# Kernel tuning notes

Measured on AMD Instinct MI355X. Metric: run time of the kernel, lower is better.

The kernel has to match this reference:

```python
import jax, jax.numpy as jnp
import numpy as np

TEMPERATURE = 0.07
N_CLASSES = 100


def setup_inputs() -> dict:
    key = jax.random.key(0)
    k1, k2 = jax.random.split(key)
    N, D = 8192, 128
    emb = jax.random.normal(k1, (N, D), dtype=jnp.float32)
    # unit-normalize so exp(sim / temperature) stays finite in fp32
    emb = emb / jnp.linalg.norm(emb, axis=1, keepdims=True)
    labels = jax.random.randint(k2, (N,), 0, N_CLASSES, dtype=jnp.int64)
    return {"embeddings": emb, "labels": labels}


def reference(embeddings, labels):
    N = embeddings.shape[0]
    dt = embeddings.dtype
    # [N, N] similarity
    sim = jnp.matmul(embeddings, embeddings.T) / TEMPERATURE
    off_diag = 1.0 - jnp.eye(N, dtype=dt)
    pos_mask = (labels[:, None] == labels[None, :]).astype(dt) * off_diag
    exp_sim = jnp.exp(sim) * off_diag  # diagonal zeroed
    positive_sum = jnp.sum(exp_sim * pos_mask, axis=1)
    total_sum = jnp.sum(exp_sim, axis=1)
    loss = -jnp.log(positive_sum / (total_sum + 1e-8) + 1e-8)
    valid = pos_mask.sum(axis=1) > 0
    cnt = jnp.sum(valid.astype(dt))
    mean_loss = jnp.where(
        cnt > 0,
        jnp.sum(jnp.where(valid, loss, jnp.zeros_like(loss))) / jnp.maximum(cnt, 1.0),
        jnp.asarray(0.0, dtype=dt),
    )
    return mean_loss
```

## Files before the change

### kernel.cpp

```cpp
#include <hip/hip_runtime.h>

#define N 8192
#define D 128
#define SCALE_A 20.6098592f
#define NBX 64
#define NBY 8
#define NBLK (NBX * NBY)

using short8  = __attribute__((ext_vector_type(8))) short;
using float4v = __attribute__((ext_vector_type(4))) float;

#if __has_builtin(__builtin_amdgcn_exp2f)
#define EXP2(x) __builtin_amdgcn_exp2f(x)
#else
#define EXP2(x) __expf((x) * 0.69314718f)
#endif

static __device__ inline unsigned int f2bf(float f) {
    union { float f; unsigned int u; } x;
    x.f = f;
    unsigned int u = x.u;
    return (u + 0x7FFFu + ((u >> 16) & 1u)) >> 16;
}

__global__ __launch_bounds__(256) void cl_prep(
    const float* __restrict__ emb, unsigned short* __restrict__ bfB,
    unsigned short* __restrict__ bfA, float* __restrict__ tot,
    int* __restrict__ ticket)
{
    const int t = blockIdx.x * 256 + threadIdx.x;
    const float* p = emb + (size_t)t * 16;
    uint4 ob[2], oa[2];
    #pragma unroll
    for (int h = 0; h < 2; ++h) {
        float4v f0 = *(const float4v*)(p + h * 8);
        float4v f1 = *(const float4v*)(p + h * 8 + 4);
        ob[h].x = f2bf(f0[0]) | (f2bf(f0[1]) << 16);
        ob[h].y = f2bf(f0[2]) | (f2bf(f0[3]) << 16);
        ob[h].z = f2bf(f1[0]) | (f2bf(f1[1]) << 16);
        ob[h].w = f2bf(f1[2]) | (f2bf(f1[3]) << 16);
        oa[h].x = f2bf(f0[0] * SCALE_A) | (f2bf(f0[1] * SCALE_A) << 16);
        oa[h].y = f2bf(f0[2] * SCALE_A) | (f2bf(f0[3] * SCALE_A) << 16);
        oa[h].z = f2bf(f1[0] * SCALE_A) | (f2bf(f1[1] * SCALE_A) << 16);
        oa[h].w = f2bf(f1[2] * SCALE_A) | (f2bf(f1[3] * SCALE_A) << 16);
    }
    ((uint4*)bfB)[t * 2]     = ob[0];
    ((uint4*)bfB)[t * 2 + 1] = ob[1];
    ((uint4*)bfA)[t * 2]     = oa[0];
    ((uint4*)bfA)[t * 2 + 1] = oa[1];
    if (t < 2 * N) tot[t] = 0.f;
    if (t == 0) *ticket = 0;
}

__global__ __launch_bounds__(256, 2) void cl_main(
    const unsigned short* __restrict__ bfA, const unsigned short* __restrict__ bfB,
    const int* __restrict__ labels,
    float* __restrict__ tot, float* __restrict__ pos,
    int* __restrict__ ticket, float* __restrict__ out)
{
    __shared__ uint4 ldsB[128 * 16];
    __shared__ float sred[2][4];
    __shared__ int s_ticket;

    const int tid  = threadIdx.x;
    const int lane = tid & 63;
    const int wave = tid >> 6;
    const int q    = lane >> 4;
    const int c    = lane & 15;
    const int rw   = blockIdx.x * 128 + wave * 32;

    short8 afrag[2][4];
    int rowlab[2][4];
    #pragma unroll
    for (int tr = 0; tr < 2; ++tr) {
        const int arow = rw + tr * 16 + c;
        #pragma unroll
        for (int ks = 0; ks < 4; ++ks)
            afrag[tr][ks] = *(const short8*)(bfA + (size_t)arow * D + ks * 32 + q * 8);
        #pragma unroll
        for (int reg = 0; reg < 4; ++reg)
            rowlab[tr][reg] = labels[rw + tr * 16 + q * 4 + reg];
    }

    float tot_a[2][4] = {{0.f,0.f,0.f,0.f},{0.f,0.f,0.f,0.f}};
    float pos_a[2][4] = {{0.f,0.f,0.f,0.f},{0.f,0.f,0.f,0.f}};

    for (int it = 0; it < 8; ++it) {
        const int cbase = blockIdx.y * 1024 + it * 128;

        const uint4* bfB4 = (const uint4*)bfB;
        #pragma unroll
        for (int i = 0; i < 8; ++i) {
            const int g     = tid + i * 256;
            const int brow  = g >> 4;
            const int chunk = g & 15;
            uint4 u = bfB4[(size_t)(cbase + brow) * 16 + chunk];
            ldsB[brow * 16 + (chunk ^ (brow & 15))] = u;
        }
        int collab[8];
        #pragma unroll
        for (int tc = 0; tc < 8; ++tc) collab[tc] = labels[cbase + tc * 16 + c];
        __syncthreads();

        float4v acc[2][8];
        #pragma unroll
        for (int tr = 0; tr < 2; ++tr)
            #pragma unroll
            for (int tc = 0; tc < 8; ++tc) {
                float4v z = {0.f, 0.f, 0.f, 0.f};
                acc[tr][tc] = z;
            }

        const short8* ldsS = (const short8*)ldsB;
        #pragma unroll
        for (int ks = 0; ks < 4; ++ks) {
            const short8* pk = ldsS + c * 16 + ((ks * 4 + q) ^ c);
            #pragma unroll
            for (int tc = 0; tc < 8; ++tc) {
                short8 b = pk[tc * 256];
                #pragma unroll
                for (int tr = 0; tr < 2; ++tr)
                    acc[tr][tc] = __builtin_amdgcn_mfma_f32_16x16x32_bf16(
                        afrag[tr][ks], b, acc[tr][tc], 0, 0, 0);
            }
        }

        #pragma unroll
        for (int tr = 0; tr < 2; ++tr) {
            const int rtile = rw + tr * 16;
            #pragma unroll
            for (int tc = 0; tc < 8; ++tc) {
                const bool diag_tile = (rtile == cbase + tc * 16);
                const int lc = collab[tc];
                #pragma unroll
                for (int reg = 0; reg < 4; ++reg) {
                    float v = EXP2(acc[tr][tc][reg]);
                    if (diag_tile && (q * 4 + reg) == c) v = 0.f;
                    tot_a[tr][reg] += v;
                    if (rowlab[tr][reg] == lc) pos_a[tr][reg] += v;
                }
            }
        }
        __syncthreads();
    }

    #pragma unroll
    for (int tr = 0; tr < 2; ++tr)
        #pragma unroll
        for (int reg = 0; reg < 4; ++reg) {
            float t = tot_a[tr][reg];
            float p = pos_a[tr][reg];
            #pragma unroll
            for (int m = 1; m < 16; m <<= 1) {
                t += __shfl_xor(t, m, 64);
                p += __shfl_xor(p, m, 64);
            }
            if (c == 0) {
                const int r = rw + tr * 16 + q * 4 + reg;
                atomicAdd(&tot[r], t);
                atomicAdd(&pos[r], p);
            }
        }

    asm volatile("s_waitcnt vmcnt(0)" ::: "memory");
    __syncthreads();
    if (tid == 0)
        s_ticket = __hip_atomic_fetch_add(ticket, 1, __ATOMIC_RELAXED,
                                          __HIP_MEMORY_SCOPE_AGENT);
    __syncthreads();
    if (s_ticket != NBLK - 1) return;

    float lsum = 0.f, lcnt = 0.f;
    #pragma unroll 4
    for (int i = tid; i < N; i += 256) {
        const float t = __hip_atomic_load(&tot[i], __ATOMIC_RELAXED,
                                          __HIP_MEMORY_SCOPE_AGENT);
        const float p = __hip_atomic_load(&pos[i], __ATOMIC_RELAXED,
                                          __HIP_MEMORY_SCOPE_AGENT);
        const float loss = -__logf(p / (t + 1e-8f) + 1e-8f);
        if (p > 0.f) { lsum += loss; lcnt += 1.f; }
    }
    #pragma unroll
    for (int m = 1; m < 64; m <<= 1) {
        lsum += __shfl_xor(lsum, m, 64);
        lcnt += __shfl_xor(lcnt, m, 64);
    }
    if (lane == 0) { sred[0][wave] = lsum; sred[1][wave] = lcnt; }
    __syncthreads();
    if (tid == 0) {
        const float s = sred[0][0] + sred[0][1] + sred[0][2] + sred[0][3];
        const float n = sred[1][0] + sred[1][1] + sred[1][2] + sred[1][3];
        out[0] = (n > 0.f) ? s / fmaxf(n, 1.f) : 0.f;
    }
}

extern "C" void kernel_launch(void* const* d_in, const int* in_sizes, int n_in,
                              void* d_out, int out_size, void* d_ws, size_t ws_size,
                              hipStream_t stream) {
    const float* emb  = (const float*)d_in[0];
    const int* labels = (const int*)d_in[1];
    unsigned short* bfB = (unsigned short*)d_ws;
    unsigned short* bfA = bfB + (size_t)N * D;
    float* tot    = (float*)(bfA + (size_t)N * D);
    float* pos    = tot + N;
    int*   ticket = (int*)(pos + N);

    cl_prep<<<256, 256, 0, stream>>>(emb, bfB, bfA, tot, ticket);
    cl_main<<<dim3(NBX, NBY), 256, 0, stream>>>(bfA, bfB, labels, tot, pos,
                                                ticket, (float*)d_out);
}
```

Baseline: 93.08 us.

## Double-buffer B tiles via direct global-to-LDS loads and stage column labels in LDS

Replaces the register round-trip B-tile staging with global_load_lds async copies into a double-buffered LDS tile, prefetching the next tile while the current one is multiplied and exponentiated. Column labels for the block's whole 1024-column span are loaded once into shared memory instead of being fetched from global every iteration. The change relies on manual vmcnt waits and raw s_barrier calls, which adds correctness risk around LDS visibility, and the extra LDS use may lower occupancy.

```diff
diff --git a/kernel.cpp b/kernel.cpp
--- a/kernel.cpp
+++ b/kernel.cpp
@@ -52,22 +52,43 @@
     if (t == 0) *ticket = 0;
 }
 
+static __device__ __forceinline__ void stage_tile(
+    const uint4* __restrict__ bfB4, int cbase, uint4* lds_dst, int tid)
+{
+    const uint4* src = bfB4 + (size_t)cbase * 16;
+    #pragma unroll
+    for (int i = 0; i < 8; ++i) {
+        const int g     = tid + i * 256;
+        const int row   = g >> 4;
+        const int chunk = g & 15;
+        __builtin_amdgcn_global_load_lds(
+            (const __attribute__((address_space(1))) void*)(src + row * 16 + (chunk ^ (row & 15))),
+            (__attribute__((address_space(3))) void*)(lds_dst + g),
+            16, 0, 0);
+    }
+}
+
 __global__ __launch_bounds__(256, 2) void cl_main(
     const unsigned short* __restrict__ bfA, const unsigned short* __restrict__ bfB,
     const int* __restrict__ labels,
     float* __restrict__ tot, float* __restrict__ pos,
     int* __restrict__ ticket, float* __restrict__ out)
 {
-    __shared__ uint4 ldsB[128 * 16];
+    __shared__ uint4 ldsB[2][128 * 16];
+    __shared__ int   s_collab[1024];
     __shared__ float sred[2][4];
-    __shared__ int s_ticket;
+    __shared__ int   s_ticket;
 
     const int tid  = threadIdx.x;
     const int lane = tid & 63;
     const int wave = tid >> 6;
     const int q    = lane >> 4;
     const int c    = lane & 15;
-    const int rw   = blockIdx.x * 128 + wave * 32;
+    const int rw     = blockIdx.x * 128 + wave * 32;
+    const int cbase0 = blockIdx.y * 1024;
+    const uint4* bfB4 = (const uint4*)bfB;
+
+    stage_tile(bfB4, cbase0, &ldsB[0][0], tid);
 
     short8 afrag[2][4];
     int rowlab[2][4];
@@ -82,25 +103,31 @@
             rowlab[tr][reg] = labels[rw + tr * 16 + q * 4 + reg];
     }
 
+    {
+        int4 lv = *(const int4*)(labels + cbase0 + tid * 4);
+        *(int4*)(&s_collab[tid * 4]) = lv;
+    }
+    asm volatile("s_waitcnt lgkmcnt(0)" ::: "memory");
+    __builtin_amdgcn_s_barrier();
+
     float tot_a[2][4] = {{0.f,0.f,0.f,0.f},{0.f,0.f,0.f,0.f}};
     float pos_a[2][4] = {{0.f,0.f,0.f,0.f},{0.f,0.f,0.f,0.f}};
 
+    int cur = 0;
+    #pragma unroll 1
     for (int it = 0; it < 8; ++it) {
-        const int cbase = blockIdx.y * 1024 + it * 128;
-
-        const uint4* bfB4 = (const uint4*)bfB;
-        #pragma unroll
-        for (int i = 0; i < 8; ++i) {
-            const int g     = tid + i * 256;
-            const int brow  = g >> 4;
-            const int chunk = g & 15;
-            uint4 u = bfB4[(size_t)(cbase + brow) * 16 + chunk];
-            ldsB[brow * 16 + (chunk ^ (brow & 15))] = u;
-        }
+        if (it < 7) {
+            stage_tile(bfB4, cbase0 + (it + 1) * 128, &ldsB[cur ^ 1][0], tid);
+            asm volatile("s_waitcnt vmcnt(8)" ::: "memory");
+        } else {
+            asm volatile("s_waitcnt vmcnt(0)" ::: "memory");
+        }
+        __builtin_amdgcn_s_barrier();
+        __builtin_amdgcn_sched_barrier(0);
+
         int collab[8];
         #pragma unroll
-        for (int tc = 0; tc < 8; ++tc) collab[tc] = labels[cbase + tc * 16 + c];
-        __syncthreads();
+        for (int tc = 0; tc < 8; ++tc) collab[tc] = s_collab[it * 128 + tc * 16 + c];
 
         float4v acc[2][8];
         #pragma unroll
@@ -111,7 +138,7 @@
                 acc[tr][tc] = z;
             }
 
-        const short8* ldsS = (const short8*)ldsB;
+        const short8* ldsS = (const short8*)&ldsB[cur][0];
         #pragma unroll
         for (int ks = 0; ks < 4; ++ks) {
             const short8* pk = ldsS + c * 16 + ((ks * 4 + q) ^ c);
@@ -125,6 +152,7 @@
             }
         }
 
+        const int cbase = cbase0 + it * 128;
         #pragma unroll
         for (int tr = 0; tr < 2; ++tr) {
             const int rtile = rw + tr * 16;
@@ -141,7 +169,10 @@
                 }
             }
         }
-        __syncthreads();
+
+        __builtin_amdgcn_sched_barrier(0);
+        __builtin_amdgcn_s_barrier();
+        cur ^= 1;
     }
 
     #pragma unroll
```

Result: no change. 93.37 us (+0.3%).

## Pre-swizzle bf16 operands into MFMA fragment layout and drop LDS staging

Applied to the files above, without the earlier changes.

The prep kernel now writes the bf16 A and B matrices in the exact per-lane MFMA fragment order, so the main kernel can load B fragments straight from global/L2 with coalesced short8 loads. The LDS tile, its swizzle and both barriers per iteration go away. The grid becomes 1024 one-dimensional blocks with 4 blocks per CU, each sweeping 32 column tiles of 16. The diagonal check moves to per-tile branches. Reuse of B drops from the whole block to a single wave, which raises L2 traffic, and the smaller accumulator set lowers per-wave ILP.

```diff
diff --git a/kernel.cpp b/kernel.cpp
--- a/kernel.cpp
+++ b/kernel.cpp
@@ -3,9 +3,8 @@
 #define N 8192
 #define D 128
 #define SCALE_A 20.6098592f
-#define NBX 64
-#define NBY 8
-#define NBLK (NBX * NBY)
+#define NBLK 1024
+#define NBLK_PREP 256
 
 using short8  = __attribute__((ext_vector_type(8))) short;
 using float4v = __attribute__((ext_vector_type(4))) float;
@@ -24,124 +23,144 @@
 }
 
 __global__ __launch_bounds__(256) void cl_prep(
-    const float* __restrict__ emb, unsigned short* __restrict__ bfB,
-    unsigned short* __restrict__ bfA, float* __restrict__ tot,
+    const float* __restrict__ emb, unsigned short* __restrict__ bfA,
+    unsigned short* __restrict__ bfB, float* __restrict__ tot,
     int* __restrict__ ticket)
 {
-    const int t = blockIdx.x * 256 + threadIdx.x;
-    const float* p = emb + (size_t)t * 16;
-    uint4 ob[2], oa[2];
-    #pragma unroll
-    for (int h = 0; h < 2; ++h) {
-        float4v f0 = *(const float4v*)(p + h * 8);
-        float4v f1 = *(const float4v*)(p + h * 8 + 4);
-        ob[h].x = f2bf(f0[0]) | (f2bf(f0[1]) << 16);
-        ob[h].y = f2bf(f0[2]) | (f2bf(f0[3]) << 16);
-        ob[h].z = f2bf(f1[0]) | (f2bf(f1[1]) << 16);
-        ob[h].w = f2bf(f1[2]) | (f2bf(f1[3]) << 16);
-        oa[h].x = f2bf(f0[0] * SCALE_A) | (f2bf(f0[1] * SCALE_A) << 16);
-        oa[h].y = f2bf(f0[2] * SCALE_A) | (f2bf(f0[3] * SCALE_A) << 16);
-        oa[h].z = f2bf(f1[0] * SCALE_A) | (f2bf(f1[1] * SCALE_A) << 16);
-        oa[h].w = f2bf(f1[2] * SCALE_A) | (f2bf(f1[3] * SCALE_A) << 16);
-    }
-    ((uint4*)bfB)[t * 2]     = ob[0];
-    ((uint4*)bfB)[t * 2 + 1] = ob[1];
-    ((uint4*)bfA)[t * 2]     = oa[0];
-    ((uint4*)bfA)[t * 2 + 1] = oa[1];
+    const int t  = blockIdx.x * 256 + threadIdx.x;
+    const int r  = t >> 3;
+    const int s  = t & 7;
+    const int ks = s >> 1;
+    const int h  = s & 1;
+    const int rt = r >> 4;
+    const int c  = r & 15;
+    const int base = (rt * 4 + ks) * 64 + h * 32 + c;
+
+    const float* p = emb + (size_t)r * D + s * 16;
+    float4v f0 = *(const float4v*)(p);
+    float4v f1 = *(const float4v*)(p + 4);
+    float4v f2 = *(const float4v*)(p + 8);
+    float4v f3 = *(const float4v*)(p + 12);
+
+    uint4 b0, b1, a0, a1;
+    b0.x = f2bf(f0[0]) | (f2bf(f0[1]) << 16);
+    b0.y = f2bf(f0[2]) | (f2bf(f0[3]) << 16);
+    b0.z = f2bf(f1[0]) | (f2bf(f1[1]) << 16);
+    b0.w = f2bf(f1[2]) | (f2bf(f1[3]) << 16);
+    b1.x = f2bf(f2[0]) | (f2bf(f2[1]) << 16);
+    b1.y = f2bf(f2[2]) | (f2bf(f2[3]) << 16);
+    b1.z = f2bf(f3[0]) | (f2bf(f3[1]) << 16);
+    b1.w = f2bf(f3[2]) | (f2bf(f3[3]) << 16);
+    a0.x = f2bf(f0[0] * SCALE_A) | (f2bf(f0[1] * SCALE_A) << 16);
+    a0.y = f2bf(f0[2] * SCALE_A) | (f2bf(f0[3] * SCALE_A) << 16);
+    a0.z = f2bf(f1[0] * SCALE_A) | (f2bf(f1[1] * SCALE_A) << 16);
+    a0.w = f2bf(f1[2] * SCALE_A) | (f2bf(f1[3] * SCALE_A) << 16);
+    a1.x = f2bf(f2[0] * SCALE_A) | (f2bf(f2[1] * SCALE_A) << 16);
+    a1.y = f2bf(f2[2] * SCALE_A) | (f2bf(f2[3] * SCALE_A) << 16);
+    a1.z = f2bf(f3[0] * SCALE_A) | (f2bf(f3[1] * SCALE_A) << 16);
+    a1.w = f2bf(f3[2] * SCALE_A) | (f2bf(f3[3] * SCALE_A) << 16);
+
+    ((uint4*)bfA)[base]      = a0;
+    ((uint4*)bfA)[base + 16] = a1;
+    ((uint4*)bfB)[base]      = b0;
+    ((uint4*)bfB)[base + 16] = b1;
+
     if (t < 2 * N) tot[t] = 0.f;
     if (t == 0) *ticket = 0;
 }
 
-__global__ __launch_bounds__(256, 2) void cl_main(
+__global__ __launch_bounds__(256, 4) void cl_main(
     const unsigned short* __restrict__ bfA, const unsigned short* __restrict__ bfB,
     const int* __restrict__ labels,
     float* __restrict__ tot, float* __restrict__ pos,
     int* __restrict__ ticket, float* __restrict__ out)
 {
-    __shared__ uint4 ldsB[128 * 16];
     __shared__ float sred[2][4];
-    __shared__ int s_ticket;
+    __shared__ int   s_ticket;
 
     const int tid  = threadIdx.x;
     const int lane = tid & 63;
     const int wave = tid >> 6;
     const int q    = lane >> 4;
     const int c    = lane & 15;
-    const int rw   = blockIdx.x * 128 + wave * 32;
+
+    const int rb = blockIdx.x & 63;
+    const int cs = blockIdx.x >> 6;
+    const int w0  = rb * 128 + wave * 32;
+    const int rt0 = w0 >> 4;
+    const int ct0 = cs * 32;
+
+    const short8* A8 = (const short8*)bfA;
+    const short8* B8 = (const short8*)bfB;
 
     short8 afrag[2][4];
     int rowlab[2][4];
     #pragma unroll
     for (int tr = 0; tr < 2; ++tr) {
-        const int arow = rw + tr * 16 + c;
         #pragma unroll
         for (int ks = 0; ks < 4; ++ks)
-            afrag[tr][ks] = *(const short8*)(bfA + (size_t)arow * D + ks * 32 + q * 8);
+            afrag[tr][ks] = A8[((rt0 + tr) * 4 + ks) * 64 + lane];
         #pragma unroll
         for (int reg = 0; reg < 4; ++reg)
-            rowlab[tr][reg] = labels[rw + tr * 16 + q * 4 + reg];
+            rowlab[tr][reg] = labels[w0 + tr * 16 + q * 4 + reg];
     }
 
     float tot_a[2][4] = {{0.f,0.f,0.f,0.f},{0.f,0.f,0.f,0.f}};
     float pos_a[2][4] = {{0.f,0.f,0.f,0.f},{0.f,0.f,0.f,0.f}};
 
-    for (int it = 0; it < 8; ++it) {
-        const int cbase = blockIdx.y * 1024 + it * 128;
-
-        const uint4* bfB4 = (const uint4*)bfB;
-        #pragma unroll
-        for (int i = 0; i < 8; ++i) {
-            const int g     = tid + i * 256;
-            const int brow  = g >> 4;
-            const int chunk = g & 15;
-            uint4 u = bfB4[(size_t)(cbase + brow) * 16 + chunk];
-            ldsB[brow * 16 + (chunk ^ (brow & 15))] = u;
+    #pragma unroll 2
+    for (int t = 0; t < 32; ++t) {
+        const int ct = ct0 + t;
+        const short8* bp = B8 + (size_t)ct * 256;
+        short8 b0 = bp[lane];
+        short8 b1 = bp[64 + lane];
+        short8 b2 = bp[128 + lane];
+        short8 b3 = bp[192 + lane];
+        const int lc = labels[ct * 16 + c];
+
+        float4v acc0 = {0.f, 0.f, 0.f, 0.f};
+        float4v acc1 = {0.f, 0.f, 0.f, 0.f};
+        acc0 = __builtin_amdgcn_mfma_f32_16x16x32_bf16(afrag[0][0], b0, acc0, 0, 0, 0);
+        acc1 = __builtin_amdgcn_mfma_f32_16x16x32_bf16(afrag[1][0], b0, acc1, 0, 0, 0);
+        acc0 = __builtin_amdgcn_mfma_f32_16x16x32_bf16(afrag[0][1], b1, acc0, 0, 0, 0);
+        acc1 = __builtin_amdgcn_mfma_f32_16x16x32_bf16(afrag[1][1], b1, acc1, 0, 0, 0);
+        acc0 = __builtin_amdgcn_mfma_f32_16x16x32_bf16(afrag[0][2], b2, acc0, 0, 0, 0);
+        acc1 = __builtin_amdgcn_mfma_f32_16x16x32_bf16(afrag[1][2], b2, acc1, 0, 0, 0);
+        acc0 = __builtin_amdgcn_mfma_f32_16x16x32_bf16(afrag[0][3], b3, acc0, 0, 0, 0);
+        acc1 = __builtin_amdgcn_mfma_f32_16x16x32_bf16(afrag[1][3], b3, acc1, 0, 0, 0);
+
+        if (ct == rt0) {
+            #pragma unroll
+            for (int reg = 0; reg < 4; ++reg) {
+                float v = EXP2(acc0[reg]);
+                if ((q * 4 + reg) == c) v = 0.f;
+                tot_a[0][reg] += v;
+                if (rowlab[0][reg] == lc) pos_a[0][reg] += v;
+            }
+        } else {
+            #pragma unroll
+            for (int reg = 0; reg < 4; ++reg) {
+                float v = EXP2(acc0[reg]);
+                tot_a[0][reg] += v;
+                if (rowlab[0][reg] == lc) pos_a[0][reg] += v;
+            }
         }
-        int collab[8];
-        #pragma unroll
-        for (int tc = 0; tc < 8; ++tc) collab[tc] = labels[cbase + tc * 16 + c];
-        __syncthreads();
-
-        float4v acc[2][8];
-        #pragma unroll
-        for (int tr = 0; tr < 2; ++tr)
-            #pragma unroll
-            for (int tc = 0; tc < 8; ++tc) {
-                float4v z = {0.f, 0.f, 0.f, 0.f};
-                acc[tr][tc] = z;
-            }
-
-        const short8* ldsS = (const short8*)ldsB;
-        #pragma unroll
-        for (int ks = 0; ks < 4; ++ks) {
-            const short8* pk = ldsS + c * 16 + ((ks * 4 + q) ^ c);
-            #pragma unroll
-            for (int tc = 0; tc < 8; ++tc) {
-                short8 b = pk[tc * 256];
-                #pragma unroll
-                for (int tr = 0; tr < 2; ++tr)
-                    acc[tr][tc] = __builtin_amdgcn_mfma_f32_16x16x32_bf16(
-                        afrag[tr][ks], b, acc[tr][tc], 0, 0, 0);
+        if (ct == rt0 + 1) {
+            #pragma unroll
+            for (int reg = 0; reg < 4; ++reg) {
+                float v = EXP2(acc1[reg]);
+                if ((q * 4 + reg) == c) v = 0.f;
+                tot_a[1][reg] += v;
+                if (rowlab[1][reg] == lc) pos_a[1][reg] += v;
+            }
+        } else {
+            #pragma unroll
+            for (int reg = 0; reg < 4; ++reg) {
+                float v = EXP2(acc1[reg]);
+                tot_a[1][reg] += v;
+                if (rowlab[1][reg] == lc) pos_a[1][reg] += v;
             }
         }
-
-        #pragma unroll
-        for (int tr = 0; tr < 2; ++tr) {
-            const int rtile = rw + tr * 16;
-            #pragma unroll
-            for (int tc = 0; tc < 8; ++tc) {
-                const bool diag_tile = (rtile == cbase + tc * 16);
-                const int lc = collab[tc];
-                #pragma unroll
-                for (int reg = 0; reg < 4; ++reg) {
-                    float v = EXP2(acc[tr][tc][reg]);
-                    if (diag_tile && (q * 4 + reg) == c) v = 0.f;
-                    tot_a[tr][reg] += v;
-                    if (rowlab[tr][reg] == lc) pos_a[tr][reg] += v;
-                }
-            }
-        }
-        __syncthreads();
     }
 
     #pragma unroll
@@ -156,7 +175,7 @@
                 p += __shfl_xor(p, m, 64);
             }
             if (c == 0) {
-                const int r = rw + tr * 16 + q * 4 + reg;
+                const int r = w0 + tr * 16 + q * 4 + reg;
                 atomicAdd(&tot[r], t);
                 atomicAdd(&pos[r], p);
             }
@@ -199,13 +218,13 @@
                               hipStream_t stream) {
     const float* emb  = (const float*)d_in[0];
     const int* labels = (const int*)d_in[1];
-    unsigned short* bfB = (unsigned short*)d_ws;
-    unsigned short* bfA = bfB + (size_t)N * D;
-    float* tot    = (float*)(bfA + (size_t)N * D);
+    unsigned short* bfA = (unsigned short*)d_ws;
+    unsigned short* bfB = bfA + (size_t)N * D;
+    float* tot    = (float*)(bfB + (size_t)N * D);
     float* pos    = tot + N;
     int*   ticket = (int*)(pos + N);
 
-    cl_prep<<<256, 256, 0, stream>>>(emb, bfB, bfA, tot, ticket);
-    cl_main<<<dim3(NBX, NBY), 256, 0, stream>>>(bfA, bfB, labels, tot, pos,
-                                                ticket, (float*)d_out);
-}
+    cl_prep<<<NBLK_PREP, 256, 0, stream>>>(emb, bfA, bfB, tot, ticket);
+    cl_main<<<NBLK, 256, 0, stream>>>(bfA, bfB, labels, tot, pos,
+                                      ticket, (float*)d_out);
+}
```

After: 98.41 us. 1.06x slower.
